# Optimization experiments

Measured on AMD Instinct MI355X. Metric: run time of the kernel, lower is better.

Reference implementation:

```python
import jax, jax.numpy as jnp
import numpy as np

B, T, IN, CELL, OUT = 512, 32, 512, 128, 128


def setup_inputs() -> dict:
    key = jax.random.key(0)
    ks = jax.random.split(key, 6)
    d = IN + CELL
    w = lambda k, shape, fan: jax.random.normal(k, shape, jnp.float32) / np.sqrt(fan).astype(np.float32)
    return {
        "x": jax.random.normal(ks[0], (B, T, IN), jnp.float32),
        "Wf": w(ks[1], (d, CELL), d), "bf": jnp.zeros((CELL,), jnp.float32),
        "Wi1": w(ks[2], (d, CELL), d), "bi1": jnp.zeros((CELL,), jnp.float32),
        "Wi2": w(ks[3], (d, CELL), d), "bi2": jnp.zeros((CELL,), jnp.float32),
        "Wo": w(ks[4], (d, CELL), d), "bo": jnp.zeros((CELL,), jnp.float32),
        "Wc": w(ks[5], (CELL, OUT), CELL), "bc": jnp.zeros((OUT,), jnp.float32),
    }


def reference(x, Wf, bf, Wi1, bi1, Wi2, bi2, Wo, bo, Wc, bc):
    # Faithful to MyLSTM.forward: loop runs x.shape[1] times; each iteration
    # concatenates the FULL [B,T,CELL] cell_state with the FULL [B,T,IN] x
    # (x is never sliced per step). Only the last iteration's output matters,
    # but we carry it through the scan to match the loop structure exactly.
    Tn = x.shape[1]
    c0 = jnp.zeros(x.shape[:2] + (Wf.shape[1],), x.dtype)
    out0 = jnp.zeros(x.shape[:2] + (Wc.shape[1],), x.dtype)

    def step(carry, _):
        c, _prev_out = carry
        inp = jnp.concatenate([c, x], axis=-1)  # [B,T,CELL+IN]
        f = jax.nn.sigmoid(inp @ Wf + bf)
        c = c * f + jax.nn.sigmoid(inp @ Wi1 + bi1) * jnp.tanh(inp @ Wi2 + bi2)
        o = jax.nn.sigmoid(inp @ Wo + bo) * jnp.tanh(c)
        out = jax.nn.softmax(o @ Wc + bc, axis=2)  # out_features != 1 branch
        return (c, out), None

    (c, out), _ = jax.lax.scan(step, (c0, out0), None, length=Tn)
    return out, c
```

## Files before the change

### kernel.cpp

```cpp
#include <hip/hip_runtime.h>
#include <stdint.h>

#define ROWS  16384
#define CELL  128
#define INF   512
#define RPB   32
#define NSTEP 32

typedef _Float16 f16x8 __attribute__((ext_vector_type(8)));
typedef _Float16 f16x4 __attribute__((ext_vector_type(4)));
typedef float    f32x4 __attribute__((ext_vector_type(4)));

#define MFMA16(a, b, c) __builtin_amdgcn_mfma_f32_16x16x32_f16((a), (b), (c), 0, 0, 0)

#define AOFF  0
#define XOFF  65536
#define WCOFF 327680
#define WSTOT 344064

#define LOG2E  1.44269504f
#define LOG2E2 2.88539008f

__device__ __forceinline__ unsigned short f2h_bits(float f) {
  _Float16 h = (_Float16)f;
  return *(unsigned short*)&h;
}
__device__ __forceinline__ float sig2(float z) {
  return __builtin_amdgcn_rcpf(1.f + __builtin_amdgcn_exp2f(-z));
}
__device__ __forceinline__ float tanh2(float z) {
  return 1.f - 2.f * __builtin_amdgcn_rcpf(__builtin_amdgcn_exp2f(z) + 1.f);
}

__global__ __launch_bounds__(256) void prep_kernel(
    const float* __restrict__ Wf, const float* __restrict__ Wi1,
    const float* __restrict__ Wi2, const float* __restrict__ Wo,
    const float* __restrict__ Wc, unsigned short* __restrict__ ws) {
  int id = blockIdx.x * blockDim.x + threadIdx.x;
  if (id >= WSTOT) return;
  const float* Wg[4] = {Wf, Wi1, Wi2, Wo};
  const float scl[4] = {LOG2E, LOG2E, LOG2E2, LOG2E};
  float v;
  int k, n, base;
  if (id < XOFF) {
    int g = id >> 14, r = id & 16383;
    k = r >> 7; n = r & 127;
    v = Wg[g][k * CELL + n] * scl[g];
    base = g * 16384;
  } else if (id < WCOFF) {
    int t = id - XOFF;
    int g = t >> 16, r = t & 65535;
    k = r >> 7; n = r & 127;
    v = Wg[g][(CELL + k) * CELL + n] * scl[g];
    base = XOFF + g * 65536;
  } else {
    int r = id - WCOFF;
    k = r >> 7; n = r & 127;
    v = Wc[k * CELL + n] * LOG2E;
    base = WCOFF;
  }
  int ks = k >> 5, kk = k & 31;
  int lane = ((kk >> 3) << 4) | (n & 15);
  int j = kk & 7, nb = n >> 4;
  ws[base + ((ks * 8 + nb) * 64 + lane) * 8 + j] = f2h_bits(v);
}

__global__ __launch_bounds__(512, 4) void lstm_kernel(
    const float* __restrict__ x,
    const float* __restrict__ bf_, const float* __restrict__ bi1,
    const float* __restrict__ bi2, const float* __restrict__ bo,
    const float* __restrict__ bc,
    const unsigned short* __restrict__ ws, float* __restrict__ out) {

  __shared__ _Float16 cF[2][32 * 128];
  __shared__ union {
    _Float16 xs[32 * 512];
    struct {
      float    ue[32][132];
      _Float16 o[32 * 128];
    } ep;
  } uS;

  const int tid  = threadIdx.x;
  const int lane = tid & 63;
  const int w    = tid >> 6;
  const int n16  = lane & 15;
  const int g4   = lane >> 4;
  const int sxor = n16 & 7;
  const int col0 = w * 16 + g4 * 4;
  const int r0   = blockIdx.x * RPB;

  const _Float16* Aw  = (const _Float16*)ws + AOFF;
  const _Float16* Xw  = (const _Float16*)ws + XOFF;
  const _Float16* Wcw = (const _Float16*)ws + WCOFF;

  int aoff[4];
#pragma unroll
  for (int ks = 0; ks < 4; ++ks)
    aoff[ks] = n16 * 128 + (((4 * ks + g4) ^ sxor) << 3);
  const int woff = n16 * 128 + (((2 * w + (g4 >> 1)) ^ sxor) << 3) + (g4 & 1) * 4;

  {
    const float* xb = x + (size_t)r0 * INF;
#pragma unroll
    for (int i = 0; i < 8; ++i) {
      int flat = tid + i * 512;
      int row = flat >> 7, c4 = flat & 127;
      const float4 v = ((const float4*)(xb + (size_t)row * INF))[c4];
      f16x4 h = {(_Float16)v.x, (_Float16)v.y, (_Float16)v.z, (_Float16)v.w};
      int idx = row * 512 + (((c4 >> 1) ^ (row & 7)) << 3) + (c4 & 1) * 4;
      *(f16x4*)&uS.xs[idx] = h;
    }
  }
  __syncthreads();

  f32x4 u[2][4];
#pragma unroll
  for (int h = 0; h < 2; ++h)
#pragma unroll
    for (int g = 0; g < 4; ++g)
#pragma unroll
      for (int i = 0; i < 4; ++i) u[h][g][i] = 0.f;

#pragma unroll 2
  for (int ks = 0; ks < 16; ++ks) {
    f16x8 b0 = *(const f16x8*)(Xw + 0 * 65536 + ((ks * 8 + w) * 64 + lane) * 8);
    f16x8 b1 = *(const f16x8*)(Xw + 1 * 65536 + ((ks * 8 + w) * 64 + lane) * 8);
    f16x8 b2 = *(const f16x8*)(Xw + 2 * 65536 + ((ks * 8 + w) * 64 + lane) * 8);
    f16x8 b3 = *(const f16x8*)(Xw + 3 * 65536 + ((ks * 8 + w) * 64 + lane) * 8);
#pragma unroll
    for (int h = 0; h < 2; ++h) {
      f16x8 a = *(const f16x8*)&uS.xs[(h * 16 + n16) * 512 +
                                      (((4 * ks + g4) ^ sxor) << 3)];
      u[h][0] = MFMA16(b0, a, u[h][0]);
      u[h][1] = MFMA16(b1, a, u[h][1]);
      u[h][2] = MFMA16(b2, a, u[h][2]);
      u[h][3] = MFMA16(b3, a, u[h][3]);
    }
  }
  {
    f32x4 b0 = *(const f32x4*)&bf_[col0];
    f32x4 b1 = *(const f32x4*)&bi1[col0];
    f32x4 b2 = *(const f32x4*)&bi2[col0];
    f32x4 b3 = *(const f32x4*)&bo[col0];
#pragma unroll
    for (int h = 0; h < 2; ++h)
#pragma unroll
      for (int i = 0; i < 4; ++i) {
        u[h][0][i] = fmaf(b0[i], LOG2E,  u[h][0][i]);
        u[h][1][i] = fmaf(b1[i], LOG2E,  u[h][1][i]);
        u[h][2][i] = fmaf(b2[i], LOG2E2, u[h][2][i]);
        u[h][3][i] = fmaf(b3[i], LOG2E,  u[h][3][i]);
      }
  }
  __syncthreads();

  *(f32x4*)&uS.ep.ue[n16][col0]      = u[0][3];
  *(f32x4*)&uS.ep.ue[16 + n16][col0] = u[1][3];

  f16x8 wr[3][4];
#pragma unroll
  for (int g = 0; g < 3; ++g)
#pragma unroll
    for (int ks = 0; ks < 4; ++ks)
      wr[g][ks] = *(const f16x8*)(Aw + g * 16384 + ((ks * 8 + w) * 64 + lane) * 8);

  f32x4 cr0, cr1;
  {
    f16x4 hv;
#pragma unroll
    for (int i = 0; i < 4; ++i) {
      float c0 = sig2(u[0][1][i]) * tanh2(u[0][2][i]);
      cr0[i] = c0;
      hv[i] = (_Float16)c0;
    }
    *(f16x4*)&cF[0][woff] = hv;
#pragma unroll
    for (int i = 0; i < 4; ++i) {
      float c0 = sig2(u[1][1][i]) * tanh2(u[1][2][i]);
      cr1[i] = c0;
      hv[i] = (_Float16)c0;
    }
    *(f16x4*)&cF[0][2048 + woff] = hv;
  }
  __syncthreads();

#pragma unroll 1
  for (int t = 1; t < NSTEP - 1; ++t) {
    const _Float16* rd = cF[(t + 1) & 1];
    _Float16*       wp = cF[t & 1];
    f16x8 a0 = *(const f16x8*)(rd + aoff[0]);
    f16x8 a1 = *(const f16x8*)(rd + aoff[1]);
    f16x8 a2 = *(const f16x8*)(rd + aoff[2]);
    f16x8 a3 = *(const f16x8*)(rd + aoff[3]);
    f32x4 zf  = MFMA16(wr[0][0], a0, u[0][0]);
    f32x4 zi1 = MFMA16(wr[1][0], a0, u[0][1]);
    f32x4 zi2 = MFMA16(wr[2][0], a0, u[0][2]);
    zf  = MFMA16(wr[0][1], a1, zf);
    zi1 = MFMA16(wr[1][1], a1, zi1);
    zi2 = MFMA16(wr[2][1], a1, zi2);
    zf  = MFMA16(wr[0][2], a2, zf);
    zi1 = MFMA16(wr[1][2], a2, zi1);
    zi2 = MFMA16(wr[2][2], a2, zi2);
    zf  = MFMA16(wr[0][3], a3, zf);
    zi1 = MFMA16(wr[1][3], a3, zi1);
    zi2 = MFMA16(wr[2][3], a3, zi2);
    f16x8 e0 = *(const f16x8*)(rd + 2048 + aoff[0]);
    f16x8 e1 = *(const f16x8*)(rd + 2048 + aoff[1]);
    f16x8 e2 = *(const f16x8*)(rd + 2048 + aoff[2]);
    f16x8 e3 = *(const f16x8*)(rd + 2048 + aoff[3]);
    {
      f16x4 hv;
#pragma unroll
      for (int i = 0; i < 4; ++i) {
        float fg = sig2(zf[i]);
        float ig = sig2(zi1[i]);
        float gg = tanh2(zi2[i]);
        float cn = fmaf(cr0[i], fg, ig * gg);
        cr0[i] = cn;
        hv[i] = (_Float16)cn;
      }
      *(f16x4*)&wp[woff] = hv;
    }
    zf  = MFMA16(wr[0][0], e0, u[1][0]);
    zi1 = MFMA16(wr[1][0], e0, u[1][1]);
    zi2 = MFMA16(wr[2][0], e0, u[1][2]);
    zf  = MFMA16(wr[0][1], e1, zf);
    zi1 = MFMA16(wr[1][1], e1, zi1);
    zi2 = MFMA16(wr[2][1], e1, zi2);
    zf  = MFMA16(wr[0][2], e2, zf);
    zi1 = MFMA16(wr[1][2], e2, zi1);
    zi2 = MFMA16(wr[2][2], e2, zi2);
    zf  = MFMA16(wr[0][3], e3, zf);
    zi1 = MFMA16(wr[1][3], e3, zi1);
    zi2 = MFMA16(wr[2][3], e3, zi2);
    {
      f16x4 hv;
#pragma unroll
      for (int i = 0; i < 4; ++i) {
        float fg = sig2(zf[i]);
        float ig = sig2(zi1[i]);
        float gg = tanh2(zi2[i]);
        float cn = fmaf(cr1[i], fg, ig * gg);
        cr1[i] = cn;
        hv[i] = (_Float16)cn;
      }
      *(f16x4*)&wp[2048 + woff] = hv;
    }
    __syncthreads();
  }

  {
    const _Float16* rd = cF[0];
    f16x8 bo0 = *(const f16x8*)(Aw + 3 * 16384 + ((0 * 8 + w) * 64 + lane) * 8);
    f16x8 bo1 = *(const f16x8*)(Aw + 3 * 16384 + ((1 * 8 + w) * 64 + lane) * 8);
    f16x8 bo2 = *(const f16x8*)(Aw + 3 * 16384 + ((2 * 8 + w) * 64 + lane) * 8);
    f16x8 bo3 = *(const f16x8*)(Aw + 3 * 16384 + ((3 * 8 + w) * 64 + lane) * 8);
#pragma unroll
    for (int h = 0; h < 2; ++h) {
      const int hoff = h * 2048;
      f16x8 a0 = *(const f16x8*)(rd + hoff + aoff[0]);
      f16x8 a1 = *(const f16x8*)(rd + hoff + aoff[1]);
      f16x8 a2 = *(const f16x8*)(rd + hoff + aoff[2]);
      f16x8 a3 = *(const f16x8*)(rd + hoff + aoff[3]);
      f32x4 zos = *(const f32x4*)&uS.ep.ue[h * 16 + n16][col0];
      f32x4 zf  = MFMA16(wr[0][0], a0, u[h][0]);
      f32x4 zi1 = MFMA16(wr[1][0], a0, u[h][1]);
      f32x4 zi2 = MFMA16(wr[2][0], a0, u[h][2]);
      f32x4 zo  = MFMA16(bo0,      a0, zos);
      zf  = MFMA16(wr[0][1], a1, zf);
      zi1 = MFMA16(wr[1][1], a1, zi1);
      zi2 = MFMA16(wr[2][1], a1, zi2);
      zo  = MFMA16(bo1,      a1, zo);
      zf  = MFMA16(wr[0][2], a2, zf);
      zi1 = MFMA16(wr[1][2], a2, zi1);
      zi2 = MFMA16(wr[2][2], a2, zi2);
      zo  = MFMA16(bo2,      a2, zo);
      zf  = MFMA16(wr[0][3], a3, zf);
      zi1 = MFMA16(wr[1][3], a3, zi1);
      zi2 = MFMA16(wr[2][3], a3, zi2);
      zo  = MFMA16(bo3,      a3, zo);
      f16x4 hv;
      f32x4& cr = h ? cr1 : cr0;
#pragma unroll
      for (int i = 0; i < 4; ++i) {
        float fg = sig2(zf[i]);
        float ig = sig2(zi1[i]);
        float gg = tanh2(zi2[i]);
        float cn = fmaf(cr[i], fg, ig * gg);
        cr[i] = cn;
        float ov = sig2(zo[i]) * tanh2(cn * LOG2E2);
        hv[i] = (_Float16)ov;
      }
      *(f16x4*)&uS.ep.o[hoff + woff] = hv;
    }
  }
  __syncthreads();

  {
    f32x4 s0, s1;
#pragma unroll
    for (int i = 0; i < 4; ++i) { s0[i] = 0.f; s1[i] = 0.f; }
#pragma unroll
    for (int ks = 0; ks < 4; ++ks) {
      f16x8 bW = *(const f16x8*)(Wcw + ((ks * 8 + w) * 64 + lane) * 8);
      f16x8 oa = *(const f16x8*)&uS.ep.o[aoff[ks]];
      f16x8 ob = *(const f16x8*)&uS.ep.o[2048 + aoff[ks]];
      s0 = MFMA16(bW, oa, s0);
      s1 = MFMA16(bW, ob, s1);
    }
    f32x4 bcv = *(const f32x4*)&bc[col0];
    f32x4 ev0, ev1;
#pragma unroll
    for (int i = 0; i < 4; ++i) {
      ev0[i] = __builtin_amdgcn_exp2f(fmaf(bcv[i], LOG2E, s0[i]));
      ev1[i] = __builtin_amdgcn_exp2f(fmaf(bcv[i], LOG2E, s1[i]));
    }
    *(f32x4*)&uS.ep.ue[n16][col0]      = ev0;
    *(f32x4*)&uS.ep.ue[16 + n16][col0] = ev1;
    __syncthreads();

#pragma unroll
    for (int rr = 0; rr < 4; ++rr) {
      int r = w * 4 + rr;
      float e0 = uS.ep.ue[r][lane];
      float e1 = uS.ep.ue[r][lane + 64];
      float sm = e0 + e1;
#pragma unroll
      for (int off = 32; off; off >>= 1) sm += __shfl_xor(sm, off, 64);
      float inv = __builtin_amdgcn_rcpf(sm);
      size_t base = (size_t)(r0 + r) * 128;
      out[base + lane]      = e0 * inv;
      out[base + lane + 64] = e1 * inv;
    }

    *(f32x4*)&out[(size_t)ROWS * 128 + (size_t)(r0 + n16) * 128 + col0] = cr0;
    *(f32x4*)&out[(size_t)ROWS * 128 + (size_t)(r0 + 16 + n16) * 128 + col0] = cr1;
  }
}

extern "C" void kernel_launch(void* const* d_in, const int* in_sizes, int n_in,
                              void* d_out, int out_size, void* d_ws, size_t ws_size,
                              hipStream_t stream) {
  const float* x   = (const float*)d_in[0];
  const float* Wf  = (const float*)d_in[1];
  const float* bf_ = (const float*)d_in[2];
  const float* Wi1 = (const float*)d_in[3];
  const float* bi1 = (const float*)d_in[4];
  const float* Wi2 = (const float*)d_in[5];
  const float* bi2 = (const float*)d_in[6];
  const float* Wo  = (const float*)d_in[7];
  const float* bo  = (const float*)d_in[8];
  const float* Wc  = (const float*)d_in[9];
  const float* bc  = (const float*)d_in[10];
  unsigned short* ws = (unsigned short*)d_ws;
  float* out = (float*)d_out;

  hipLaunchKernelGGL(prep_kernel, dim3((WSTOT + 255) / 256), dim3(256), 0, stream,
                     Wf, Wi1, Wi2, Wo, Wc, ws);
  hipLaunchKernelGGL(lstm_kernel, dim3(ROWS / RPB), dim3(512), 0, stream,
                     x, bf_, bi1, bi2, bo, bc, ws, out);
}
```

Baseline: 167.9 us.

## Software-pipeline LSTM recurrence across two row halves with ping-pong buffers

After: 171.7 us. 1.02x slower.

```diff
diff --git a/kernel.cpp b/kernel.cpp
--- a/kernel.cpp
+++ b/kernel.cpp
@@ -65,14 +65,15 @@
   ws[base + ((ks * 8 + nb) * 64 + lane) * 8 + j] = f2h_bits(v);
 }
 
-__global__ __launch_bounds__(512, 4) void lstm_kernel(
+__global__ __launch_bounds__(512, 2) void lstm_kernel(
     const float* __restrict__ x,
     const float* __restrict__ bf_, const float* __restrict__ bi1,
     const float* __restrict__ bi2, const float* __restrict__ bo,
     const float* __restrict__ bc,
     const unsigned short* __restrict__ ws, float* __restrict__ out) {
 
-  __shared__ _Float16 cF[2][32 * 128];
+  __shared__ _Float16 cTA[16 * 128];
+  __shared__ _Float16 cTB[16 * 128];
   __shared__ union {
     _Float16 xs[32 * 512];
     struct {
@@ -174,95 +175,76 @@
       cr0[i] = c0;
       hv[i] = (_Float16)c0;
     }
-    *(f16x4*)&cF[0][woff] = hv;
+    *(f16x4*)&cTA[woff] = hv;
 #pragma unroll
     for (int i = 0; i < 4; ++i) {
       float c0 = sig2(u[1][1][i]) * tanh2(u[1][2][i]);
       cr1[i] = c0;
       hv[i] = (_Float16)c0;
     }
-    *(f16x4*)&cF[0][2048 + woff] = hv;
-  }
+    *(f16x4*)&cTB[woff] = hv;
+  }
+  __syncthreads();
+
+#define RDQ(BUF) \
+  a0 = *(const f16x8*)((BUF) + aoff[0]); \
+  a1 = *(const f16x8*)((BUF) + aoff[1]); \
+  a2 = *(const f16x8*)((BUF) + aoff[2]); \
+  a3 = *(const f16x8*)((BUF) + aoff[3]);
+
+#define MML(Z0, Z1, Z2, U0, U1, U2) \
+  Z0 = MFMA16(wr[0][0], a0, U0); Z1 = MFMA16(wr[1][0], a0, U1); Z2 = MFMA16(wr[2][0], a0, U2); \
+  Z0 = MFMA16(wr[0][1], a1, Z0); Z1 = MFMA16(wr[1][1], a1, Z1); Z2 = MFMA16(wr[2][1], a1, Z2); \
+  Z0 = MFMA16(wr[0][2], a2, Z0); Z1 = MFMA16(wr[1][2], a2, Z1); Z2 = MFMA16(wr[2][2], a2, Z2); \
+  Z0 = MFMA16(wr[0][3], a3, Z0); Z1 = MFMA16(wr[1][3], a3, Z1); Z2 = MFMA16(wr[2][3], a3, Z2);
+
+#define GWQ(Z0, Z1, Z2, CR, BUF) { \
+  f16x4 hv; \
+  _Pragma("unroll") \
+  for (int i = 0; i < 4; ++i) { \
+    float fg = sig2(Z0[i]); \
+    float ig = sig2(Z1[i]); \
+    float gg = tanh2(Z2[i]); \
+    float cn = fmaf(CR[i], fg, ig * gg); \
+    CR[i] = cn; \
+    hv[i] = (_Float16)cn; \
+  } \
+  *(f16x4*)&(BUF)[woff] = hv; }
+
+  f16x8 a0, a1, a2, a3;
+  f32x4 zfA, ziA, zgA, zfB, ziB, zgB;
+
+  RDQ(cTA)
+  MML(zfA, ziA, zgA, u[0][0], u[0][1], u[0][2])
   __syncthreads();
 
 #pragma unroll 1
-  for (int t = 1; t < NSTEP - 1; ++t) {
-    const _Float16* rd = cF[(t + 1) & 1];
-    _Float16*       wp = cF[t & 1];
-    f16x8 a0 = *(const f16x8*)(rd + aoff[0]);
-    f16x8 a1 = *(const f16x8*)(rd + aoff[1]);
-    f16x8 a2 = *(const f16x8*)(rd + aoff[2]);
-    f16x8 a3 = *(const f16x8*)(rd + aoff[3]);
-    f32x4 zf  = MFMA16(wr[0][0], a0, u[0][0]);
-    f32x4 zi1 = MFMA16(wr[1][0], a0, u[0][1]);
-    f32x4 zi2 = MFMA16(wr[2][0], a0, u[0][2]);
-    zf  = MFMA16(wr[0][1], a1, zf);
-    zi1 = MFMA16(wr[1][1], a1, zi1);
-    zi2 = MFMA16(wr[2][1], a1, zi2);
-    zf  = MFMA16(wr[0][2], a2, zf);
-    zi1 = MFMA16(wr[1][2], a2, zi1);
-    zi2 = MFMA16(wr[2][2], a2, zi2);
-    zf  = MFMA16(wr[0][3], a3, zf);
-    zi1 = MFMA16(wr[1][3], a3, zi1);
-    zi2 = MFMA16(wr[2][3], a3, zi2);
-    f16x8 e0 = *(const f16x8*)(rd + 2048 + aoff[0]);
-    f16x8 e1 = *(const f16x8*)(rd + 2048 + aoff[1]);
-    f16x8 e2 = *(const f16x8*)(rd + 2048 + aoff[2]);
-    f16x8 e3 = *(const f16x8*)(rd + 2048 + aoff[3]);
-    {
-      f16x4 hv;
-#pragma unroll
-      for (int i = 0; i < 4; ++i) {
-        float fg = sig2(zf[i]);
-        float ig = sig2(zi1[i]);
-        float gg = tanh2(zi2[i]);
-        float cn = fmaf(cr0[i], fg, ig * gg);
-        cr0[i] = cn;
-        hv[i] = (_Float16)cn;
-      }
-      *(f16x4*)&wp[woff] = hv;
-    }
-    zf  = MFMA16(wr[0][0], e0, u[1][0]);
-    zi1 = MFMA16(wr[1][0], e0, u[1][1]);
-    zi2 = MFMA16(wr[2][0], e0, u[1][2]);
-    zf  = MFMA16(wr[0][1], e1, zf);
-    zi1 = MFMA16(wr[1][1], e1, zi1);
-    zi2 = MFMA16(wr[2][1], e1, zi2);
-    zf  = MFMA16(wr[0][2], e2, zf);
-    zi1 = MFMA16(wr[1][2], e2, zi1);
-    zi2 = MFMA16(wr[2][2], e2, zi2);
-    zf  = MFMA16(wr[0][3], e3, zf);
-    zi1 = MFMA16(wr[1][3], e3, zi1);
-    zi2 = MFMA16(wr[2][3], e3, zi2);
-    {
-      f16x4 hv;
-#pragma unroll
-      for (int i = 0; i < 4; ++i) {
-        float fg = sig2(zf[i]);
-        float ig = sig2(zi1[i]);
-        float gg = tanh2(zi2[i]);
-        float cn = fmaf(cr1[i], fg, ig * gg);
-        cr1[i] = cn;
-        hv[i] = (_Float16)cn;
-      }
-      *(f16x4*)&wp[2048 + woff] = hv;
-    }
+  for (int s = 1; s < 30; ++s) {
+    RDQ(cTB)
+    GWQ(zfA, ziA, zgA, cr0, cTA)
+    MML(zfB, ziB, zgB, u[1][0], u[1][1], u[1][2])
     __syncthreads();
-  }
-
-  {
-    const _Float16* rd = cF[0];
+    RDQ(cTA)
+    GWQ(zfB, ziB, zgB, cr1, cTB)
+    MML(zfA, ziA, zgA, u[0][0], u[0][1], u[0][2])
+    __syncthreads();
+  }
+  RDQ(cTB)
+  GWQ(zfA, ziA, zgA, cr0, cTA)
+  MML(zfB, ziB, zgB, u[1][0], u[1][1], u[1][2])
+  __syncthreads();
+  GWQ(zfB, ziB, zgB, cr1, cTB)
+  __syncthreads();
+
+  {
     f16x8 bo0 = *(const f16x8*)(Aw + 3 * 16384 + ((0 * 8 + w) * 64 + lane) * 8);
     f16x8 bo1 = *(const f16x8*)(Aw + 3 * 16384 + ((1 * 8 + w) * 64 + lane) * 8);
     f16x8 bo2 = *(const f16x8*)(Aw + 3 * 16384 + ((2 * 8 + w) * 64 + lane) * 8);
     f16x8 bo3 = *(const f16x8*)(Aw + 3 * 16384 + ((3 * 8 + w) * 64 + lane) * 8);
 #pragma unroll
     for (int h = 0; h < 2; ++h) {
-      const int hoff = h * 2048;
-      f16x8 a0 = *(const f16x8*)(rd + hoff + aoff[0]);
-      f16x8 a1 = *(const f16x8*)(rd + hoff + aoff[1]);
-      f16x8 a2 = *(const f16x8*)(rd + hoff + aoff[2]);
-      f16x8 a3 = *(const f16x8*)(rd + hoff + aoff[3]);
+      const _Float16* rd = h ? cTB : cTA;
+      RDQ(rd)
       f32x4 zos = *(const f32x4*)&uS.ep.ue[h * 16 + n16][col0];
       f32x4 zf  = MFMA16(wr[0][0], a0, u[h][0]);
       f32x4 zi1 = MFMA16(wr[1][0], a0, u[h][1]);
@@ -292,7 +274,7 @@
         float ov = sig2(zo[i]) * tanh2(cn * LOG2E2);
         hv[i] = (_Float16)ov;
       }
-      *(f16x4*)&uS.ep.o[hoff + woff] = hv;
+      *(f16x4*)&uS.ep.o[h * 2048 + woff] = hv;
     }
   }
   __syncthreads();
```
